# Performance work log

Measured on AMD Instinct MI355X. Metric: run time of the kernel, lower is better.

## Reference

```python
import jax, jax.numpy as jnp
import numpy as np

B, S, H, NUM_P = 32, 1024, 768, 49
P2 = NUM_P * 2


def setup_inputs() -> dict:
    key = jax.random.key(0)
    ks = jax.random.split(key, 8)
    hidden_states = jax.random.normal(ks[0], (B, S, H), dtype=jnp.float32)
    batch_subject_ids = jax.random.randint(ks[1], (B, 2), 0, S, dtype=jnp.int32)
    input_mask = jax.random.randint(ks[2], (B, S), 0, 2, dtype=jnp.int32)
    attn_w = jax.random.normal(ks[3], (1, H), dtype=jnp.float32) * 0.02
    attn_b = jnp.zeros((1,), dtype=jnp.float32)
    gate_w = jax.random.normal(ks[4], (H, 2 * H), dtype=jnp.float32) * 0.02
    gate_b = jnp.zeros((H,), dtype=jnp.float32)
    lin_w = jax.random.normal(ks[5], (P2, H), dtype=jnp.float32) * 0.02
    lin_b = jnp.zeros((P2,), dtype=jnp.float32)
    return {
        'hidden_states': hidden_states,
        'batch_subject_ids': batch_subject_ids,
        'input_mask': input_mask,
        'attn_w': attn_w,
        'attn_b': attn_b,
        'gate_w': gate_w,
        'gate_b': gate_b,
        'lin_w': lin_w,
        'lin_b': lin_b,
    }


def reference(hidden_states, batch_subject_ids, input_mask, attn_w, attn_b,
              gate_w, gate_b, lin_w, lin_b):
    # NOTE: the torch module computes s = h[s_start] + h[s_end] from
    # batch_subject_ids but never uses it -> dead code, omitted.
    # Dropout(p=0.4) is treated in eval mode (identity).
    b, s, h = hidden_states.shape
    # cue_len per batch, clamped to [1, S] as in the torch code
    cue_len = jnp.clip(jnp.sum(input_mask, axis=-1), 1, s)            # [B]
    valid = jnp.arange(s)[None, :] < cue_len[:, None]                 # [B,S] bool

    # attention pooling over the first cue_len tokens
    scores = jnp.einsum('bsh,oh->bso', hidden_states, attn_w) + attn_b  # [B,S,1]
    scores = jnp.where(valid[..., None], scores, -jnp.inf)
    attn = jax.nn.softmax(scores, axis=1)                             # [B,S,1]
    s_x = jnp.sum(attn * hidden_states, axis=1)                       # [B,H]

    # gate(cat([s_x, h_i])) split into the two halves of gate_w
    gate_ws = gate_w[:, :h]   # acts on s_x
    gate_wh = gate_w[:, h:]   # acts on h_i
    g_logit = (jnp.einsum('bh,oh->bo', s_x, gate_ws)[:, None, :]
               + jnp.einsum('bsh,oh->bso', hidden_states, gate_wh)
               + gate_b)                                              # [B,S,H]
    g = jax.nn.sigmoid(g_logit)
    fused = g * s_x[:, None, :] + (1.0 - g) * hidden_states           # [B,S,H]
    all_s = jnp.where(valid[..., None], fused, 0.0)                   # zeros beyond cue_len

    hs = hidden_states + all_s
    out = jax.nn.sigmoid(jnp.einsum('bsh,oh->bso', hs, lin_w) + lin_b)
    eps = 1e-7
    return jnp.clip(out, eps, 1.0 - eps)                              # [B,S,2*num_p]
```

## Files before the change

kernel.cpp:

```cpp
#include <hip/hip_runtime.h>
#include <hip/hip_bf16.h>
#include <cstdint>

#define NB 32
#define NS 1024
#define NH 768
#define NP 98

typedef __attribute__((ext_vector_type(8))) short short8;
typedef __attribute__((ext_vector_type(4))) float f32x4;

static __device__ __forceinline__ ushort f2bf(float f) {
  uint32_t u = __builtin_bit_cast(uint32_t, f);
  u += 0x7fff + ((u >> 16) & 1);
  return (ushort)(u >> 16);
}
static __device__ __forceinline__ float bf2f(ushort h) {
  uint32_t u = ((uint32_t)h) << 16;
  return __builtin_bit_cast(float, u);
}
static __device__ __forceinline__ void gload16(const ushort* g, ushort* l) {
  __builtin_amdgcn_global_load_lds((const __attribute__((address_space(1))) uint32_t*)g,
                                   (__attribute__((address_space(3))) uint32_t*)l, 16, 0, 0);
}

__global__ void k_wprep(const float* __restrict__ gate_w, const float* __restrict__ lin_w,
                        ushort* __restrict__ wh_bf, ushort* __restrict__ lin_bf) {
  int r = blockIdx.x, t = threadIdx.x;
  if (r < NH) {
    float4 v = *(const float4*)(gate_w + (size_t)r * (2 * NH) + NH + t * 4);
    ushort4 h;
    h.x = f2bf(v.x); h.y = f2bf(v.y); h.z = f2bf(v.z); h.w = f2bf(v.w);
    *(ushort4*)&wh_bf[(size_t)r * NH + t * 4] = h;
  } else {
    int n = r - NH;
    ushort4 h; h.x = 0; h.y = 0; h.z = 0; h.w = 0;
    if (n < NP) {
      float4 v = *(const float4*)(lin_w + (size_t)n * NH + t * 4);
      h.x = f2bf(v.x); h.y = f2bf(v.y); h.z = f2bf(v.z); h.w = f2bf(v.w);
    }
    *(ushort4*)&lin_bf[(size_t)n * NH + t * 4] = h;
  }
}

__global__ void k_prep(const float* __restrict__ hidden, const float* __restrict__ aw,
                       const float* __restrict__ ab, ushort* __restrict__ hid_bf,
                       float* __restrict__ scores) {
  int wid = threadIdx.x >> 6, lane = threadIdx.x & 63;
  int rbase = blockIdx.x * 32 + wid * 8;
  float w0[12];
#pragma unroll
  for (int j = 0; j < 3; ++j) {
    float4 wv = *(const float4*)(aw + j * 256 + lane * 4);
    w0[4 * j] = wv.x; w0[4 * j + 1] = wv.y; w0[4 * j + 2] = wv.z; w0[4 * j + 3] = wv.w;
  }
  float abv = ab[0];
  for (int r = rbase; r < rbase + 8; ++r) {
    const float* row = hidden + (size_t)r * NH;
    float acc = 0.f;
#pragma unroll
    for (int j = 0; j < 3; ++j) {
      float4 v = *(const float4*)(row + j * 256 + lane * 4);
      acc += v.x * w0[4 * j] + v.y * w0[4 * j + 1] + v.z * w0[4 * j + 2] + v.w * w0[4 * j + 3];
      ushort4 h;
      h.x = f2bf(v.x); h.y = f2bf(v.y); h.z = f2bf(v.z); h.w = f2bf(v.w);
      *(ushort4*)&hid_bf[(size_t)r * NH + j * 256 + lane * 4] = h;
    }
#pragma unroll
    for (int off = 32; off; off >>= 1) acc += __shfl_xor(acc, off);
    if (lane == 0) scores[r] = acc + abv;
  }
}

__global__ void k_stats(const int* __restrict__ mask, const float* __restrict__ scores,
                        int* __restrict__ cue, float* __restrict__ mout,
                        float* __restrict__ lout) {
  int b = blockIdx.x, t = threadIdx.x;
  int lane = t & 63, w = t >> 6;
  __shared__ float red[4];
  __shared__ int redi[4];
  __shared__ int cue_s;

  int sm = 0;
#pragma unroll
  for (int i = 0; i < 4; ++i) sm += mask[b * NS + t + 256 * i];
#pragma unroll
  for (int off = 32; off; off >>= 1) sm += __shfl_xor(sm, off);
  if (lane == 0) redi[w] = sm;
  __syncthreads();
  if (t == 0) {
    int tot = redi[0] + redi[1] + redi[2] + redi[3];
    tot = min(max(tot, 1), NS);
    cue_s = tot;
    cue[b] = tot;
  }
  __syncthreads();
  int cl = cue_s;

  float mx = -1e30f;
#pragma unroll
  for (int i = 0; i < 4; ++i) {
    int s = t + 256 * i;
    if (s < cl) mx = fmaxf(mx, scores[b * NS + s]);
  }
#pragma unroll
  for (int off = 32; off; off >>= 1) mx = fmaxf(mx, __shfl_xor(mx, off));
  if (lane == 0) red[w] = mx;
  __syncthreads();
  float m = fmaxf(fmaxf(red[0], red[1]), fmaxf(red[2], red[3]));
  __syncthreads();

  float sum = 0.f;
#pragma unroll
  for (int i = 0; i < 4; ++i) {
    int s = t + 256 * i;
    if (s < cl) sum += __expf(scores[b * NS + s] - m);
  }
#pragma unroll
  for (int off = 32; off; off >>= 1) sum += __shfl_xor(sum, off);
  if (lane == 0) red[w] = sum;
  __syncthreads();
  if (t == 0) {
    mout[b] = m;
    lout[b] = red[0] + red[1] + red[2] + red[3];
  }
}

__global__ void k_sx(const ushort* __restrict__ hid_bf, const float* __restrict__ scores,
                     const int* __restrict__ cue, const float* __restrict__ m,
                     const float* __restrict__ l, float* __restrict__ sx) {
  int b = blockIdx.y, ch = blockIdx.x, t = threadIdx.x;
  int s0 = ch * 64;
  int cl = cue[b];
  if (s0 >= cl) return;
  __shared__ float w[64];
  if (t < 64) {
    int s = s0 + t;
    float wv = 0.f;
    if (s < cl) wv = __expf(scores[b * NS + s] - m[b]) / l[b];
    w[t] = wv;
  }
  __syncthreads();
  float4 a; a.x = 0.f; a.y = 0.f; a.z = 0.f; a.w = 0.f;
  const ushort* base = hid_bf + ((size_t)(b * NS + s0)) * NH;
  for (int s = 0; s < 64; ++s) {
    float ws = w[s];
    ushort4 v = *(const ushort4*)(base + s * NH + t * 4);
    a.x = fmaf(ws, bf2f(v.x), a.x);
    a.y = fmaf(ws, bf2f(v.y), a.y);
    a.z = fmaf(ws, bf2f(v.z), a.z);
    a.w = fmaf(ws, bf2f(v.w), a.w);
  }
  float* dst = sx + b * NH + t * 4;
  atomicAdd(dst + 0, a.x);
  atomicAdd(dst + 1, a.y);
  atomicAdd(dst + 2, a.z);
  atomicAdd(dst + 3, a.w);
}

__global__ void k_g1(const float* __restrict__ sx, const float* __restrict__ gate_w,
                     float* __restrict__ g1) {
  int b = blockIdx.y, og = blockIdx.x, t = threadIdx.x;
  __shared__ float sl[NH];
  if (t < 192) *(float4*)&sl[t * 4] = *(const float4*)(sx + b * NH + t * 4);
  __syncthreads();
  int w = t >> 6, lane = t & 63;
#pragma unroll 4
  for (int j = 0; j < 32; ++j) {
    int o = og * 128 + w * 32 + j;
    const float* gr = gate_w + (size_t)o * (2 * NH);
    float acc = 0.f;
#pragma unroll
    for (int q = 0; q < 3; ++q) {
      float4 gv = *(const float4*)(gr + q * 256 + lane * 4);
      float4 sv = *(const float4*)(&sl[q * 256 + lane * 4]);
      acc += gv.x * sv.x + gv.y * sv.y + gv.z * sv.z + gv.w * sv.w;
    }
#pragma unroll
    for (int off = 32; off; off >>= 1) acc += __shfl_xor(acc, off);
    if (lane == 0) g1[b * NH + o] = acc;
  }
}

__global__ __launch_bounds__(256, 2) void k_gemm1(
    const ushort* __restrict__ hid_bf, const ushort* __restrict__ wh_bf,
    const float* __restrict__ gate_b, const float* __restrict__ sx,
    const float* __restrict__ g1, const int* __restrict__ cue,
    ushort* __restrict__ hs_bf) {
  __shared__ ushort As[128 * 32];
  __shared__ ushort Bs[192 * 32];
  const int t = threadIdx.x;
  const int lane = t & 63, wid = t >> 6;
  const int half = lane >> 4, r16 = lane & 15;

  const int bid = blockIdx.x;
  const int xcd = bid & 7, i = bid >> 3;
  const int nt = i & 3, mt = xcd * 32 + (i >> 2);
  const int row0 = mt * 128, col0 = nt * 192;

  const int c0 = t, c1 = t + 256, c2 = t + 512;
  const ushort* gA0 = hid_bf + (size_t)(row0 + (c0 >> 2)) * NH + (c0 & 3) * 8;
  const ushort* gA1 = hid_bf + (size_t)(row0 + (c1 >> 2)) * NH + (c1 & 3) * 8;
  const ushort* gB0 = wh_bf + (size_t)(col0 + (c0 >> 2)) * NH + (c0 & 3) * 8;
  const ushort* gB1 = wh_bf + (size_t)(col0 + (c1 >> 2)) * NH + (c1 & 3) * 8;
  const ushort* gB2 = wh_bf + (size_t)(col0 + (c2 >> 2)) * NH + (c2 & 3) * 8;
  ushort* lA0 = &As[c0 * 8];
  ushort* lA1 = &As[c1 * 8];
  ushort* lB0 = &Bs[c0 * 8];
  ushort* lB1 = &Bs[c1 * 8];
  ushort* lB2 = &Bs[c2 * 8];

  const int wm = wid >> 1, wn = wid & 1;
  f32x4 acc[4][6];
#pragma unroll
  for (int mf = 0; mf < 4; ++mf)
#pragma unroll
    for (int nf = 0; nf < 6; ++nf) acc[mf][nf] = (f32x4)0.f;

  for (int ks = 0; ks < 24; ++ks) {
    const int k0 = ks * 32;
    gload16(gA0 + k0, lA0);
    gload16(gA1 + k0, lA1);
    gload16(gB0 + k0, lB0);
    gload16(gB1 + k0, lB1);
    gload16(gB2 + k0, lB2);
    __syncthreads();
    short8 af[4], bfr[6];
#pragma unroll
    for (int mf = 0; mf < 4; ++mf)
      af[mf] = *(const short8*)&As[(wm * 64 + mf * 16 + r16) * 32 + half * 8];
#pragma unroll
    for (int nf = 0; nf < 6; ++nf)
      bfr[nf] = *(const short8*)&Bs[(wn * 96 + nf * 16 + r16) * 32 + half * 8];
#pragma unroll
    for (int nf = 0; nf < 6; ++nf)
#pragma unroll
      for (int mf = 0; mf < 4; ++mf)
        acc[mf][nf] = __builtin_amdgcn_mfma_f32_16x16x32_bf16(af[mf], bfr[nf], acc[mf][nf], 0, 0, 0);
    __syncthreads();
  }

  const int b = mt >> 3;
  const int cl = cue[b];
#pragma unroll
  for (int nf = 0; nf < 6; ++nf) {
    int col = col0 + wn * 96 + nf * 16 + r16;
    float g1v = g1[b * NH + col];
    float sxv = sx[b * NH + col];
    float gbv = gate_b[col];
#pragma unroll
    for (int mf = 0; mf < 4; ++mf) {
#pragma unroll
      for (int p = 0; p < 4; ++p) {
        int grow = row0 + wm * 64 + mf * 16 + half * 4 + p;
        float x = bf2f(hid_bf[(size_t)grow * NH + col]);
        float gl = g1v + acc[mf][nf][p] + gbv;
        float g = 1.f / (1.f + __expf(-gl));
        float fused = g * sxv + (1.f - g) * x;
        float hs = x + (((grow & 1023) < cl) ? fused : 0.f);
        hs_bf[(size_t)grow * NH + col] = f2bf(hs);
      }
    }
  }
}

__global__ __launch_bounds__(256, 1) void k_gemm2(
    const ushort* __restrict__ hs_bf, const ushort* __restrict__ lin_bf,
    const float* __restrict__ lin_b, float* __restrict__ out) {
  __shared__ ushort As[128 * 32];
  __shared__ ushort Bs[128 * 32];
  const int t = threadIdx.x;
  const int lane = t & 63, wid = t >> 6;
  const int half = lane >> 4, r16 = lane & 15;
  const int row0 = blockIdx.x * 128;

  const int c0 = t, c1 = t + 256;
  const ushort* gA0 = hs_bf + (size_t)(row0 + (c0 >> 2)) * NH + (c0 & 3) * 8;
  const ushort* gA1 = hs_bf + (size_t)(row0 + (c1 >> 2)) * NH + (c1 & 3) * 8;
  const ushort* gB0 = lin_bf + (size_t)(c0 >> 2) * NH + (c0 & 3) * 8;
  const ushort* gB1 = lin_bf + (size_t)(c1 >> 2) * NH + (c1 & 3) * 8;
  ushort* lA0 = &As[c0 * 8];
  ushort* lA1 = &As[c1 * 8];
  ushort* lB0 = &Bs[c0 * 8];
  ushort* lB1 = &Bs[c1 * 8];

  f32x4 acc[2][7];
#pragma unroll
  for (int mf = 0; mf < 2; ++mf)
#pragma unroll
    for (int nf = 0; nf < 7; ++nf) acc[mf][nf] = (f32x4)0.f;

  for (int ks = 0; ks < 24; ++ks) {
    const int k0 = ks * 32;
    gload16(gA0 + k0, lA0);
    gload16(gA1 + k0, lA1);
    gload16(gB0 + k0, lB0);
    gload16(gB1 + k0, lB1);
    __syncthreads();
    short8 af[2], bfr[7];
#pragma unroll
    for (int mf = 0; mf < 2; ++mf)
      af[mf] = *(const short8*)&As[(wid * 32 + mf * 16 + r16) * 32 + half * 8];
#pragma unroll
    for (int nf = 0; nf < 7; ++nf)
      bfr[nf] = *(const short8*)&Bs[(nf * 16 + r16) * 32 + half * 8];
#pragma unroll
    for (int nf = 0; nf < 7; ++nf)
#pragma unroll
      for (int mf = 0; mf < 2; ++mf)
        acc[mf][nf] = __builtin_amdgcn_mfma_f32_16x16x32_bf16(af[mf], bfr[nf], acc[mf][nf], 0, 0, 0);
    __syncthreads();
  }

#pragma unroll
  for (int nf = 0; nf < 7; ++nf) {
    int col = nf * 16 + r16;
    bool valid = col < NP;
    float lbv = valid ? lin_b[col] : 0.f;
#pragma unroll
    for (int mf = 0; mf < 2; ++mf) {
#pragma unroll
      for (int p = 0; p < 4; ++p) {
        int grow = row0 + wid * 32 + mf * 16 + half * 4 + p;
        float v = acc[mf][nf][p] + lbv;
        v = 1.f / (1.f + __expf(-v));
        v = fminf(fmaxf(v, 1e-7f), 1.f - 1e-7f);
        if (valid) out[(size_t)grow * NP + col] = v;
      }
    }
  }
}

extern "C" void kernel_launch(void* const* d_in, const int* in_sizes, int n_in,
                              void* d_out, int out_size, void* d_ws, size_t ws_size,
                              hipStream_t stream) {
  const float* hidden = (const float*)d_in[0];
  const int* mask = (const int*)d_in[2];
  const float* attn_w = (const float*)d_in[3];
  const float* attn_b = (const float*)d_in[4];
  const float* gate_w = (const float*)d_in[5];
  const float* gate_b = (const float*)d_in[6];
  const float* lin_w = (const float*)d_in[7];
  const float* lin_b = (const float*)d_in[8];
  float* out = (float*)d_out;

  float* F = (float*)d_ws;
  int* cue = (int*)F;
  float* m = F + 32;
  float* l = F + 64;
  float* scores = F + 96;
  float* sx = scores + NB * NS;
  float* g1 = sx + NB * NH;
  ushort* wh_bf = (ushort*)(g1 + NB * NH);
  ushort* lin_bf = wh_bf + (size_t)NH * NH;
  ushort* hid_bf = lin_bf + (size_t)128 * NH;
  ushort* hs_bf = hid_bf + (size_t)NB * NS * NH;

  hipMemsetAsync(sx, 0, NB * NH * sizeof(float), stream);
  k_wprep<<<896, 192, 0, stream>>>(gate_w, lin_w, wh_bf, lin_bf);
  k_prep<<<1024, 256, 0, stream>>>(hidden, attn_w, attn_b, hid_bf, scores);
  k_stats<<<NB, 256, 0, stream>>>(mask, scores, cue, m, l);
  k_sx<<<dim3(16, NB), 192, 0, stream>>>(hid_bf, scores, cue, m, l, sx);
  k_g1<<<dim3(6, NB), 256, 0, stream>>>(sx, gate_w, g1);
  k_gemm1<<<1024, 256, 0, stream>>>(hid_bf, wh_bf, gate_b, sx, g1, cue, hs_bf);
  k_gemm2<<<256, 256, 0, stream>>>(hs_bf, lin_bf, lin_b, out);
}
```

Before: 353.3 us.

## Double-buffer LDS in both GEMMs and halve gemm2 row tile

Both GEMM kernels switch to double-buffered LDS tiles, so the global-to-LDS loads for the next K step are issued before the MFMA work on the current step, aiming to hide load latency. gemm1's launch bound occupancy hint is raised from 2 to 4 blocks. gemm2 drops to 64-row tiles with 512 blocks and a hint of 4 blocks, for more parallelism across CUs. The double buffering doubles LDS per block, and the higher occupancy target may push register limits on gemm1's 96-float accumulator set, risking spills.

```diff
diff --git a/kernel.cpp b/kernel.cpp
--- a/kernel.cpp
+++ b/kernel.cpp
@@ -182,13 +182,13 @@
   }
 }
 
-__global__ __launch_bounds__(256, 2) void k_gemm1(
+__global__ __launch_bounds__(256, 4) void k_gemm1(
     const ushort* __restrict__ hid_bf, const ushort* __restrict__ wh_bf,
     const float* __restrict__ gate_b, const float* __restrict__ sx,
     const float* __restrict__ g1, const int* __restrict__ cue,
     ushort* __restrict__ hs_bf) {
-  __shared__ ushort As[128 * 32];
-  __shared__ ushort Bs[192 * 32];
+  __shared__ ushort As[2][128 * 32];
+  __shared__ ushort Bs[2][192 * 32];
   const int t = threadIdx.x;
   const int lane = t & 63, wid = t >> 6;
   const int half = lane >> 4, r16 = lane & 15;
@@ -204,11 +204,6 @@
   const ushort* gB0 = wh_bf + (size_t)(col0 + (c0 >> 2)) * NH + (c0 & 3) * 8;
   const ushort* gB1 = wh_bf + (size_t)(col0 + (c1 >> 2)) * NH + (c1 & 3) * 8;
   const ushort* gB2 = wh_bf + (size_t)(col0 + (c2 >> 2)) * NH + (c2 & 3) * 8;
-  ushort* lA0 = &As[c0 * 8];
-  ushort* lA1 = &As[c1 * 8];
-  ushort* lB0 = &Bs[c0 * 8];
-  ushort* lB1 = &Bs[c1 * 8];
-  ushort* lB2 = &Bs[c2 * 8];
 
   const int wm = wid >> 1, wn = wid & 1;
   f32x4 acc[4][6];
@@ -217,26 +212,39 @@
 #pragma unroll
     for (int nf = 0; nf < 6; ++nf) acc[mf][nf] = (f32x4)0.f;
 
-  for (int ks = 0; ks < 24; ++ks) {
-    const int k0 = ks * 32;
-    gload16(gA0 + k0, lA0);
-    gload16(gA1 + k0, lA1);
-    gload16(gB0 + k0, lB0);
-    gload16(gB1 + k0, lB1);
-    gload16(gB2 + k0, lB2);
+#define STAGE1(BUF, KS)                                  \
+  {                                                      \
+    const int k0_ = (KS) * 32;                           \
+    gload16(gA0 + k0_, &As[BUF][c0 * 8]);                \
+    gload16(gA1 + k0_, &As[BUF][c1 * 8]);                \
+    gload16(gB0 + k0_, &Bs[BUF][c0 * 8]);                \
+    gload16(gB1 + k0_, &Bs[BUF][c1 * 8]);                \
+    gload16(gB2 + k0_, &Bs[BUF][c2 * 8]);                \
+  }
+
+#define COMPUTE1(BUF)                                                             \
+  {                                                                               \
+    short8 af[4], bfr[6];                                                         \
+    _Pragma("unroll") for (int mf = 0; mf < 4; ++mf)                              \
+        af[mf] = *(const short8*)&As[BUF][(wm * 64 + mf * 16 + r16) * 32 + half * 8]; \
+    _Pragma("unroll") for (int nf = 0; nf < 6; ++nf)                              \
+        bfr[nf] = *(const short8*)&Bs[BUF][(wn * 96 + nf * 16 + r16) * 32 + half * 8]; \
+    _Pragma("unroll") for (int nf = 0; nf < 6; ++nf)                              \
+        _Pragma("unroll") for (int mf = 0; mf < 4; ++mf)                          \
+            acc[mf][nf] = __builtin_amdgcn_mfma_f32_16x16x32_bf16(af[mf], bfr[nf], \
+                                                                  acc[mf][nf], 0, 0, 0); \
+  }
+
+  STAGE1(0, 0);
+  __syncthreads();
+#pragma unroll 1
+  for (int ks2 = 0; ks2 < 12; ++ks2) {
+    const int ks = ks2 * 2;
+    STAGE1(1, ks + 1);
+    COMPUTE1(0);
     __syncthreads();
-    short8 af[4], bfr[6];
-#pragma unroll
-    for (int mf = 0; mf < 4; ++mf)
-      af[mf] = *(const short8*)&As[(wm * 64 + mf * 16 + r16) * 32 + half * 8];
-#pragma unroll
-    for (int nf = 0; nf < 6; ++nf)
-      bfr[nf] = *(const short8*)&Bs[(wn * 96 + nf * 16 + r16) * 32 + half * 8];
-#pragma unroll
-    for (int nf = 0; nf < 6; ++nf)
-#pragma unroll
-      for (int mf = 0; mf < 4; ++mf)
-        acc[mf][nf] = __builtin_amdgcn_mfma_f32_16x16x32_bf16(af[mf], bfr[nf], acc[mf][nf], 0, 0, 0);
+    if (ks + 2 < 24) STAGE1(0, ks + 2);
+    COMPUTE1(1);
     __syncthreads();
   }
 
@@ -262,53 +270,57 @@
       }
     }
   }
-}
-
-__global__ __launch_bounds__(256, 1) void k_gemm2(
+#undef STAGE1
+#undef COMPUTE1
+}
+
+__global__ __launch_bounds__(256, 4) void k_gemm2(
     const ushort* __restrict__ hs_bf, const ushort* __restrict__ lin_bf,
     const float* __restrict__ lin_b, float* __restrict__ out) {
-  __shared__ ushort As[128 * 32];
-  __shared__ ushort Bs[128 * 32];
+  __shared__ ushort As[2][64 * 32];
+  __shared__ ushort Bs[2][128 * 32];
   const int t = threadIdx.x;
   const int lane = t & 63, wid = t >> 6;
   const int half = lane >> 4, r16 = lane & 15;
-  const int row0 = blockIdx.x * 128;
-
-  const int c0 = t, c1 = t + 256;
-  const ushort* gA0 = hs_bf + (size_t)(row0 + (c0 >> 2)) * NH + (c0 & 3) * 8;
-  const ushort* gA1 = hs_bf + (size_t)(row0 + (c1 >> 2)) * NH + (c1 & 3) * 8;
-  const ushort* gB0 = lin_bf + (size_t)(c0 >> 2) * NH + (c0 & 3) * 8;
-  const ushort* gB1 = lin_bf + (size_t)(c1 >> 2) * NH + (c1 & 3) * 8;
-  ushort* lA0 = &As[c0 * 8];
-  ushort* lA1 = &As[c1 * 8];
-  ushort* lB0 = &Bs[c0 * 8];
-  ushort* lB1 = &Bs[c1 * 8];
-
-  f32x4 acc[2][7];
-#pragma unroll
-  for (int mf = 0; mf < 2; ++mf)
-#pragma unroll
-    for (int nf = 0; nf < 7; ++nf) acc[mf][nf] = (f32x4)0.f;
-
-  for (int ks = 0; ks < 24; ++ks) {
-    const int k0 = ks * 32;
-    gload16(gA0 + k0, lA0);
-    gload16(gA1 + k0, lA1);
-    gload16(gB0 + k0, lB0);
-    gload16(gB1 + k0, lB1);
+  const int row0 = blockIdx.x * 64;
+
+  const int cA = t;
+  const int cB0 = t, cB1 = t + 256;
+  const ushort* gA = hs_bf + (size_t)(row0 + (cA >> 2)) * NH + (cA & 3) * 8;
+  const ushort* gB0 = lin_bf + (size_t)(cB0 >> 2) * NH + (cB0 & 3) * 8;
+  const ushort* gB1 = lin_bf + (size_t)(cB1 >> 2) * NH + (cB1 & 3) * 8;
+
+  f32x4 acc[7];
+#pragma unroll
+  for (int nf = 0; nf < 7; ++nf) acc[nf] = (f32x4)0.f;
+
+#define STAGE2(BUF, KS)                                  \
+  {                                                      \
+    const int k0_ = (KS) * 32;                           \
+    gload16(gA + k0_, &As[BUF][cA * 8]);                 \
+    gload16(gB0 + k0_, &Bs[BUF][cB0 * 8]);               \
+    gload16(gB1 + k0_, &Bs[BUF][cB1 * 8]);               \
+  }
+
+#define COMPUTE2(BUF)                                                          \
+  {                                                                            \
+    short8 a = *(const short8*)&As[BUF][(wid * 16 + r16) * 32 + half * 8];     \
+    _Pragma("unroll") for (int nf = 0; nf < 7; ++nf) {                         \
+      short8 bv = *(const short8*)&Bs[BUF][(nf * 16 + r16) * 32 + half * 8];   \
+      acc[nf] = __builtin_amdgcn_mfma_f32_16x16x32_bf16(a, bv, acc[nf], 0, 0, 0); \
+    }                                                                          \
+  }
+
+  STAGE2(0, 0);
+  __syncthreads();
+#pragma unroll 1
+  for (int ks2 = 0; ks2 < 12; ++ks2) {
+    const int ks = ks2 * 2;
+    STAGE2(1, ks + 1);
+    COMPUTE2(0);
     __syncthreads();
-    short8 af[2], bfr[7];
-#pragma unroll
-    for (int mf = 0; mf < 2; ++mf)
-      af[mf] = *(const short8*)&As[(wid * 32 + mf * 16 + r16) * 32 + half * 8];
-#pragma unroll
-    for (int nf = 0; nf < 7; ++nf)
-      bfr[nf] = *(const short8*)&Bs[(nf * 16 + r16) * 32 + half * 8];
-#pragma unroll
-    for (int nf = 0; nf < 7; ++nf)
-#pragma unroll
-      for (int mf = 0; mf < 2; ++mf)
-        acc[mf][nf] = __builtin_amdgcn_mfma_f32_16x16x32_bf16(af[mf], bfr[nf], acc[mf][nf], 0, 0, 0);
+    if (ks + 2 < 24) STAGE2(0, ks + 2);
+    COMPUTE2(1);
     __syncthreads();
   }
 
@@ -318,17 +330,16 @@
     bool valid = col < NP;
     float lbv = valid ? lin_b[col] : 0.f;
 #pragma unroll
-    for (int mf = 0; mf < 2; ++mf) {
-#pragma unroll
-      for (int p = 0; p < 4; ++p) {
-        int grow = row0 + wid * 32 + mf * 16 + half * 4 + p;
-        float v = acc[mf][nf][p] + lbv;
-        v = 1.f / (1.f + __expf(-v));
-        v = fminf(fmaxf(v, 1e-7f), 1.f - 1e-7f);
-        if (valid) out[(size_t)grow * NP + col] = v;
-      }
-    }
-  }
+    for (int p = 0; p < 4; ++p) {
+      int grow = row0 + wid * 16 + half * 4 + p;
+      float v = acc[nf][p] + lbv;
+      v = 1.f / (1.f + __expf(-v));
+      v = fminf(fmaxf(v, 1e-7f), 1.f - 1e-7f);
+      if (valid) out[(size_t)grow * NP + col] = v;
+    }
+  }
+#undef STAGE2
+#undef COMPUTE2
 }
 
 extern "C" void kernel_launch(void* const* d_in, const int* in_sizes, int n_in,
@@ -363,5 +374,5 @@
   k_sx<<<dim3(16, NB), 192, 0, stream>>>(hid_bf, scores, cue, m, l, sx);
   k_g1<<<dim3(6, NB), 256, 0, stream>>>(sx, gate_w, g1);
   k_gemm1<<<1024, 256, 0, stream>>>(hid_bf, wh_bf, gate_b, sx, g1, cue, hs_bf);
-  k_gemm2<<<256, 256, 0, stream>>>(hs_bf, lin_bf, lin_b, out);
-}
+  k_gemm2<<<512, 256, 0, stream>>>(hs_bf, lin_bf, lin_b, out);
+}
```

Result: slower. 379.9 us (+7.5%).
